# Kernel tuning notes

Measured on AMD Instinct MI355X. Metric: run time of the kernel, lower is better.

## Reference

```python
import jax, jax.numpy as jnp
import numpy as np

N_NODES = 50000
N_EDGES = 800000
D_IN = 128
D_HID = 128


def _sage_conv(x, src, dst, W_l, b_l, W_r, num_nodes):
    # PyG SAGEConv (mean aggr): out = lin_l(mean_{j in N(i)} x_j) + lin_r(x_i)
    msgs = x[src]  # [E, d] irregular gather
    agg = jax.ops.segment_sum(msgs, dst, num_segments=num_nodes)  # [N, d]
    cnt = jax.ops.segment_sum(jnp.ones((dst.shape[0], 1), x.dtype), dst, num_segments=num_nodes)
    agg = agg / jnp.maximum(cnt, 1.0)  # mean over in-neighbors
    return agg @ W_l.T + b_l + x @ W_r.T


def setup_inputs() -> dict:
    key = jax.random.key(0)
    ks = jax.random.split(key, 8)
    x = jax.random.normal(ks[0], (N_NODES, D_IN), dtype=jnp.float32)
    edge_index = jax.random.randint(ks[1], (2, N_EDGES), 0, N_NODES, dtype=jnp.int64)
    s0 = 1.0 / np.sqrt(D_IN)
    s1 = 1.0 / np.sqrt(D_HID)
    return {
        "x": x,
        "edge_index": edge_index,
        "W_l0": jax.random.uniform(ks[2], (D_HID, D_IN), jnp.float32, -s0, s0),
        "b_l0": jnp.zeros((D_HID,), jnp.float32),
        "W_r0": jax.random.uniform(ks[3], (D_HID, D_IN), jnp.float32, -s0, s0),
        "W_l1": jax.random.uniform(ks[4], (D_HID, D_HID), jnp.float32, -s1, s1),
        "b_l1": jnp.zeros((D_HID,), jnp.float32),
        "W_r1": jax.random.uniform(ks[5], (D_HID, D_HID), jnp.float32, -s1, s1),
    }


def reference(x, edge_index, W_l0, b_l0, W_r0, W_l1, b_l1, W_r1):
    src, dst = edge_index[0], edge_index[1]
    n = x.shape[0]
    # layer 0 + ReLU (dropout is identity at inference)
    h = _sage_conv(x, src, dst, W_l0, b_l0, W_r0, n)
    h = jax.nn.relu(h)
    # layer 1 (no activation on last layer)
    out = _sage_conv(h, src, dst, W_l1, b_l1, W_r1, n)
    return out
```

## Files before the change

### kernel.cpp

```cpp
#include <hip/hip_runtime.h>


typedef __attribute__((ext_vector_type(8))) short short8;
typedef __attribute__((ext_vector_type(4))) float f32x4;

#define DEV __device__ __forceinline__

DEV unsigned short f2b(float f) {
  unsigned u = __builtin_bit_cast(unsigned, f);
  u += 0x7fffu + ((u >> 16) & 1u);
  return (unsigned short)(u >> 16);
}
DEV float b2f(unsigned short h) {
  unsigned u = ((unsigned)h) << 16;
  return __builtin_bit_cast(float, u);
}

constexpr int N_NODES = 50000;
constexpr int N_EDGES = 800000;
constexpr int D = 128;
constexpr int NBUCK = (N_NODES + 255) / 256;
constexpr int BCAP = 5120;
constexpr int NBIN = 784;
constexpr int EPB = (N_EDGES + NBIN - 1) / NBIN;
constexpr int NCONV = (N_NODES * D / 4) / 256;
constexpr int NPREP = (2 * 32 * 128) / 256;

__global__ __launch_bounds__(256) void setup_kernel(
    const float* __restrict__ x, unsigned short* __restrict__ xb,
    const float* __restrict__ Wl0, const float* __restrict__ Wr0,
    const float* __restrict__ Wl1, const float* __restrict__ Wr1,
    unsigned short* __restrict__ Bf,
    const int* __restrict__ src, const int* __restrict__ dst,
    int* __restrict__ g_bcnt, unsigned* __restrict__ staging) {
  __shared__ int cnt[NBUCK];
  __shared__ int cur[NBUCK];
  int bid = blockIdx.x;
  int t = threadIdx.x;

  if (bid < NBIN) {
    for (int i = t; i < NBUCK; i += 256) cnt[i] = 0;
    __syncthreads();
    int beg = bid * EPB;
    int end = min(beg + EPB, N_EDGES);
    for (int e = beg + t; e < end; e += 256) {
      atomicAdd(&cnt[dst[e] >> 8], 1);
    }
    __syncthreads();
    for (int i = t; i < NBUCK; i += 256) {
      cur[i] = atomicAdd(&g_bcnt[i], cnt[i]);
    }
    __syncthreads();
    for (int e = beg + t; e < end; e += 256) {
      int d = dst[e];
      int b = d >> 8;
      int p = atomicAdd(&cur[b], 1);
      if (p >= BCAP) p = BCAP - 1;
      staging[b * BCAP + p] = ((unsigned)(d & 255) << 16) | (unsigned)src[e];
    }
    return;
  }
  if (bid < NBIN + NCONV) {
    int i = (bid - NBIN) * 256 + t;
    f32x4 v = ((const f32x4*)x)[i];
    uint2 o;
    o.x = (unsigned)f2b(v.x) | ((unsigned)f2b(v.y) << 16);
    o.y = (unsigned)f2b(v.z) | ((unsigned)f2b(v.w) << 16);
    ((uint2*)xb)[i] = o;
    return;
  }
  int f = (bid - NBIN - NCONV) * 256 + t;
  int layer = f >> 12;
  int kchunk = (f >> 7) & 31;
  int n = f & 127;
  const float* W;
  if (layer == 0) W = (kchunk < 16) ? Wl0 : Wr0;
  else            W = (kchunk < 16) ? Wl1 : Wr1;
  int k = (kchunk & 15) * 8;
  const f32x4* row = (const f32x4*)(W + n * D + k);
  f32x4 a = row[0], b = row[1];
  uint4 pk;
  pk.x = (unsigned)f2b(a.x) | ((unsigned)f2b(a.y) << 16);
  pk.y = (unsigned)f2b(a.z) | ((unsigned)f2b(a.w) << 16);
  pk.z = (unsigned)f2b(b.x) | ((unsigned)f2b(b.y) << 16);
  pk.w = (unsigned)f2b(b.z) | ((unsigned)f2b(b.w) << 16);
  *(uint4*)(Bf + (size_t)f * 8) = pk;
}

__global__ __launch_bounds__(1024) void fill2_kernel(const unsigned* __restrict__ staging,
                                                     const int* __restrict__ g_bcnt,
                                                     int* __restrict__ offs,
                                                     int* __restrict__ csr) {
  __shared__ int cnts[256];
  __shared__ int tmp[256];
  __shared__ int hist[256];
  __shared__ int cur[256];
  __shared__ int sh_n, sh_bb;
  int b = blockIdx.x;
  int t = threadIdx.x;
  if (t < 256) {
    int c = (t < NBUCK) ? g_bcnt[t] : 0;
    cnts[t] = c;
    tmp[t] = c;
    hist[t] = 0;
  }
  __syncthreads();
  if (t < 256) {
    for (int off = 1; off < 256; off <<= 1) {
      int u = (t >= off) ? tmp[t - off] : 0;
      __syncthreads();
      tmp[t] += u;
      __syncthreads();
    }
  } else {
    for (int off = 1; off < 256; off <<= 1) { __syncthreads(); __syncthreads(); }
  }
  if (t == 0) {
    sh_n = cnts[b];
    sh_bb = tmp[b] - cnts[b];
  }
  __syncthreads();
  int n = sh_n;
  int bb = sh_bb;
  if (b == 0 && t == 0) offs[N_NODES] = N_EDGES;

  const unsigned* st = staging + b * BCAP;
  for (int e = t; e < n; e += 1024) atomicAdd(&hist[st[e] >> 16], 1);
  __syncthreads();
  if (t < 256) {
    int v = hist[t];
    tmp[t] = v;
    __syncthreads();
    for (int off = 1; off < 256; off <<= 1) {
      int u = (t >= off) ? tmp[t - off] : 0;
      __syncthreads();
      tmp[t] += u;
      __syncthreads();
    }
    int excl = tmp[t] - v;
    int node = b * 256 + t;
    if (node < N_NODES) offs[node] = bb + excl;
    cur[t] = bb + excl;
  } else {
    __syncthreads();
    for (int off = 1; off < 256; off <<= 1) { __syncthreads(); __syncthreads(); }
  }
  __syncthreads();
  for (int e = t; e < n; e += 1024) {
    unsigned pk = st[e];
    int p = atomicAdd(&cur[pk >> 16], 1);
    csr[p] = (int)(pk & 0xffffu);
  }
}

__global__ __launch_bounds__(256) void agg_kernel(
    const unsigned short* __restrict__ feat,
    const int* __restrict__ csr_src,
    const int* __restrict__ offs,
    unsigned short* __restrict__ out) {
  int w = (int)((blockIdx.x * blockDim.x + threadIdx.x) >> 6);
  int lane = threadIdx.x & 63;
  if (w >= N_NODES) return;
  int s = offs[w], e = offs[w + 1];
  const unsigned* f = (const unsigned*)feat;
  float ax = 0.f, ay = 0.f;
  for (int c = s; c < e; c += 64) {
    int nch = e - c;
    if (nch > 64) nch = 64;
    int idx = 0;
    if (lane < nch) idx = csr_src[c + lane];
    for (int kb = 0; kb < nch; kb += 8) {
      unsigned u[8];
#pragma unroll
      for (int j = 0; j < 8; ++j) {
        int sj = __builtin_amdgcn_readlane(idx, (kb + j) & 63);
        u[j] = f[(unsigned)sj * 64u + lane];
      }
#pragma unroll
      for (int j = 0; j < 8; ++j) {
        if (kb + j < nch) {
          ax += b2f((unsigned short)u[j]);
          ay += b2f((unsigned short)(u[j] >> 16));
        }
      }
    }
  }
  float inv = 1.0f / (float)max(e - s, 1);
  unsigned o = (unsigned)f2b(ax * inv) | ((unsigned)f2b(ay * inv) << 16);
  ((unsigned*)out)[w * 64 + lane] = o;
}

__global__ __launch_bounds__(256) void gemm_kernel(
    const unsigned short* __restrict__ Aagg,
    const unsigned short* __restrict__ Afeat,
    const unsigned short* __restrict__ Bf,
    const float* __restrict__ bias,
    float* __restrict__ out_f32,
    unsigned short* __restrict__ out_bf16,
    int relu_bf16) {
  int wave = threadIdx.x >> 6;
  int lane = threadIdx.x & 63;
  int ml = lane & 15;
  int quad = lane >> 4;
  int node0 = blockIdx.x * 64 + wave * 16;

  int arow = node0 + ml;
  if (arow >= N_NODES) arow = N_NODES - 1;

  f32x4 acc[8];
#pragma unroll
  for (int t = 0; t < 8; ++t) acc[t] = (f32x4){0.f, 0.f, 0.f, 0.f};

  const short8* bf8 = (const short8*)Bf;
#pragma unroll
  for (int mat = 0; mat < 2; ++mat) {
    const unsigned short* A = mat ? Afeat : Aagg;
    const short8* arow8 = (const short8*)(A + (size_t)arow * D);
    int kbase = mat * 16;
#pragma unroll
    for (int kc = 0; kc < 4; ++kc) {
      short8 af = arow8[kc * 4 + quad];
      int kchunk = kbase + kc * 4 + quad;
      const short8* brow = bf8 + kchunk * 128;
#pragma unroll
      for (int nt = 0; nt < 8; ++nt) {
        short8 bfr = brow[nt * 16 + ml];
        acc[nt] = __builtin_amdgcn_mfma_f32_16x16x32_bf16(af, bfr, acc[nt], 0, 0, 0);
      }
    }
  }

#pragma unroll
  for (int nt = 0; nt < 8; ++nt) {
    int col = nt * 16 + ml;
    float bv = bias[col];
#pragma unroll
    for (int r = 0; r < 4; ++r) {
      int node = node0 + quad * 4 + r;
      if (node >= N_NODES) continue;
      float v = acc[nt][r] + bv;
      if (relu_bf16) {
        v = v > 0.f ? v : 0.f;
        out_bf16[(size_t)node * D + col] = f2b(v);
      } else {
        out_f32[(size_t)node * D + col] = v;
      }
    }
  }
}

extern "C" void kernel_launch(void* const* d_in, const int* in_sizes, int n_in,
                              void* d_out, int out_size, void* d_ws, size_t ws_size,
                              hipStream_t stream) {
  const float* x   = (const float*)d_in[0];
  const int*   ei  = (const int*)d_in[1];
  const float* Wl0 = (const float*)d_in[2];
  const float* bl0 = (const float*)d_in[3];
  const float* Wr0 = (const float*)d_in[4];
  const float* Wl1 = (const float*)d_in[5];
  const float* bl1 = (const float*)d_in[6];
  const float* Wr1 = (const float*)d_in[7];
  float* out = (float*)d_out;

  char* ws = (char*)d_ws;
  size_t o = 0;
  auto carve = [&](size_t bytes) {
    char* p = ws + o;
    o += bytes;
    o = (o + 255) & ~(size_t)255;
    return p;
  };
  int* offs       = (int*)carve((size_t)(N_NODES + 1) * 4);
  int* csr        = (int*)carve((size_t)N_EDGES * 4);
  int* g_bcnt     = (int*)carve((size_t)NBUCK * 4);
  unsigned* staging = (unsigned*)carve((size_t)NBUCK * BCAP * 4);
  unsigned short* Bf   = (unsigned short*)carve((size_t)2 * 32 * 128 * 8 * 2);
  unsigned short* xb   = (unsigned short*)carve((size_t)N_NODES * D * 2);
  unsigned short* aggb = (unsigned short*)carve((size_t)N_NODES * D * 2);
  unsigned short* hb   = (unsigned short*)carve((size_t)N_NODES * D * 2);

  const int* srcp = ei;
  const int* dstp = ei + N_EDGES;

  hipMemsetAsync(g_bcnt, 0, (size_t)NBUCK * 4, stream);
  setup_kernel<<<NBIN + NCONV + NPREP, 256, 0, stream>>>(
      x, xb, Wl0, Wr0, Wl1, Wr1, Bf, srcp, dstp, g_bcnt, staging);
  fill2_kernel<<<NBUCK, 1024, 0, stream>>>(staging, g_bcnt, offs, csr);

  const int GEMM_BLOCKS = (N_NODES + 63) / 64;
  agg_kernel<<<(N_NODES + 3) / 4, 256, 0, stream>>>(xb, csr, offs, aggb);
  gemm_kernel<<<GEMM_BLOCKS, 256, 0, stream>>>(aggb, xb, Bf, bl0, nullptr, hb, 1);
  agg_kernel<<<(N_NODES + 3) / 4, 256, 0, stream>>>(hb, csr, offs, aggb);
  gemm_kernel<<<GEMM_BLOCKS, 256, 0, stream>>>(aggb, hb, Bf + 32 * 128 * 8, bl1,
                                               out, nullptr, 0);
}
```

Before: 215.7 us.

## Make aggregation persistent with grid-stride nodes and prefetched CSR indices

The aggregation kernel now runs a fixed grid of 2048 blocks. Each wave loops over nodes with a stride, prefetching the next node's offsets and neighbor indices while it processes the current node. The first 64-neighbor chunk is gathered 16 rows at a time, and source indices are clamped into range so loads past the node's degree stay safe. The goal is to hide the latency of the index and offset loads and to spend less on wave launches, at the cost of extra speculative loads and more register pressure.

```diff
diff --git a/kernel.cpp b/kernel.cpp
--- a/kernel.cpp
+++ b/kernel.cpp
@@ -25,6 +25,9 @@
 constexpr int EPB = (N_EDGES + NBIN - 1) / NBIN;
 constexpr int NCONV = (N_NODES * D / 4) / 256;
 constexpr int NPREP = (2 * 32 * 128) / 256;
+
+constexpr int AGG_BLOCKS = 2048;
+constexpr int AGG_WAVES = AGG_BLOCKS * 4;
 
 __global__ __launch_bounds__(256) void setup_kernel(
     const float* __restrict__ x, unsigned short* __restrict__ xb,
@@ -158,36 +161,76 @@
     const int* __restrict__ csr_src,
     const int* __restrict__ offs,
     unsigned short* __restrict__ out) {
-  int w = (int)((blockIdx.x * blockDim.x + threadIdx.x) >> 6);
+  int gw = (blockIdx.x << 2) + (threadIdx.x >> 6);
   int lane = threadIdx.x & 63;
-  if (w >= N_NODES) return;
-  int s = offs[w], e = offs[w + 1];
+  if (gw >= N_NODES) return;
   const unsigned* f = (const unsigned*)feat;
-  float ax = 0.f, ay = 0.f;
-  for (int c = s; c < e; c += 64) {
-    int nch = e - c;
-    if (nch > 64) nch = 64;
-    int idx = 0;
-    if (lane < nch) idx = csr_src[c + lane];
-    for (int kb = 0; kb < nch; kb += 8) {
-      unsigned u[8];
-#pragma unroll
-      for (int j = 0; j < 8; ++j) {
-        int sj = __builtin_amdgcn_readlane(idx, (kb + j) & 63);
-        u[j] = f[(unsigned)sj * 64u + lane];
-      }
-#pragma unroll
-      for (int j = 0; j < 8; ++j) {
+
+  int wA = gw;
+  int sA = offs[wA];
+  int eA = offs[wA + 1];
+  int wB = wA + AGG_WAVES;
+  bool hasB = (wB < N_NODES);
+  int sB = 0, eB = 0;
+  if (hasB) { sB = offs[wB]; eB = offs[wB + 1]; }
+  int idxA = csr_src[sA + lane];
+
+  while (true) {
+    int wC = wB + AGG_WAVES;
+    int sC = 0, eC = 0;
+    if (wC < N_NODES) { sC = offs[wC]; eC = offs[wC + 1]; }
+    int idxB = 0;
+    if (hasB) idxB = csr_src[sB + lane];
+
+    float ax = 0.f, ay = 0.f;
+    int degA = eA - sA;
+    int nch = degA > 64 ? 64 : degA;
+    for (int kb = 0; kb < nch; kb += 16) {
+      unsigned u[16];
+#pragma unroll
+      for (int j = 0; j < 16; ++j) {
+        unsigned sj = (unsigned)__builtin_amdgcn_readlane(idxA, (kb + j) & 63);
+        sj = (sj < (unsigned)N_NODES) ? sj : 0u;
+        u[j] = f[(sj << 6) + lane];
+      }
+#pragma unroll
+      for (int j = 0; j < 16; ++j) {
         if (kb + j < nch) {
           ax += b2f((unsigned short)u[j]);
           ay += b2f((unsigned short)(u[j] >> 16));
         }
       }
     }
-  }
-  float inv = 1.0f / (float)max(e - s, 1);
-  unsigned o = (unsigned)f2b(ax * inv) | ((unsigned)f2b(ay * inv) << 16);
-  ((unsigned*)out)[w * 64 + lane] = o;
+    for (int c = sA + 64; c < eA; c += 64) {
+      int nn = eA - c;
+      if (nn > 64) nn = 64;
+      int idx2 = (lane < nn) ? csr_src[c + lane] : 0;
+      for (int kb = 0; kb < nn; kb += 8) {
+        unsigned u[8];
+#pragma unroll
+        for (int j = 0; j < 8; ++j) {
+          unsigned sj = (unsigned)__builtin_amdgcn_readlane(idx2, (kb + j) & 63);
+          sj = (sj < (unsigned)N_NODES) ? sj : 0u;
+          u[j] = f[(sj << 6) + lane];
+        }
+#pragma unroll
+        for (int j = 0; j < 8; ++j) {
+          if (kb + j < nn) {
+            ax += b2f((unsigned short)u[j]);
+            ay += b2f((unsigned short)(u[j] >> 16));
+          }
+        }
+      }
+    }
+    float inv = 1.0f / (float)max(degA, 1);
+    unsigned o = (unsigned)f2b(ax * inv) | ((unsigned)f2b(ay * inv) << 16);
+    ((unsigned*)out)[(size_t)wA * 64 + lane] = o;
+
+    if (!hasB) break;
+    wA = wB; sA = sB; eA = eB; idxA = idxB;
+    wB = wC; sB = sC; eB = eC;
+    hasB = (wB < N_NODES);
+  }
 }
 
 __global__ __launch_bounds__(256) void gemm_kernel(
@@ -288,9 +331,9 @@
   fill2_kernel<<<NBUCK, 1024, 0, stream>>>(staging, g_bcnt, offs, csr);
 
   const int GEMM_BLOCKS = (N_NODES + 63) / 64;
-  agg_kernel<<<(N_NODES + 3) / 4, 256, 0, stream>>>(xb, csr, offs, aggb);
+  agg_kernel<<<AGG_BLOCKS, 256, 0, stream>>>(xb, csr, offs, aggb);
   gemm_kernel<<<GEMM_BLOCKS, 256, 0, stream>>>(aggb, xb, Bf, bl0, nullptr, hb, 1);
-  agg_kernel<<<(N_NODES + 3) / 4, 256, 0, stream>>>(hb, csr, offs, aggb);
+  agg_kernel<<<AGG_BLOCKS, 256, 0, stream>>>(hb, csr, offs, aggb);
   gemm_kernel<<<GEMM_BLOCKS, 256, 0, stream>>>(aggb, hb, Bf + 32 * 128 * 8, bl1,
                                                out, nullptr, 0);
 }
```

After: 228.7 us. +6.0%, slower.
